# Kernel optimization log

Measured on AMD Instinct MI355X. Metric: run time of the kernel, lower is better.

## Reference

```python
import jax, jax.numpy as jnp
import numpy as np

D_MODEL = 2560
NUM_HEADS = 32
NUM_KV_HEADS = 8
HEAD_DIM = 128
ROPE_THETA = 5e6
EPS = 1e-6
G = NUM_KV_HEADS
Q_PER_KV = NUM_HEADS // NUM_KV_HEADS


def setup_inputs() -> dict:
    key = jax.random.key(0)
    ks = jax.random.split(key, 5)
    B, S = 1, 2048
    scale = 0.02
    return {
        "x": jax.random.normal(ks[0], (B, S, D_MODEL), jnp.float32),
        "Wq": jax.random.normal(ks[1], (NUM_HEADS * HEAD_DIM, D_MODEL), jnp.float32) * scale,
        "Wk": jax.random.normal(ks[2], (NUM_KV_HEADS * HEAD_DIM, D_MODEL), jnp.float32) * scale,
        "Wv": jax.random.normal(ks[3], (NUM_KV_HEADS * HEAD_DIM, D_MODEL), jnp.float32) * scale,
        "Wo": jax.random.normal(ks[4], (D_MODEL, NUM_HEADS * HEAD_DIM), jnp.float32) * scale,
        "q_norm_w": jnp.ones((HEAD_DIM,), jnp.float32),
        "k_norm_w": jnp.ones((HEAD_DIM,), jnp.float32),
    }


def _rms_norm(x, w):
    var = jnp.mean(jnp.square(x), axis=-1, keepdims=True)
    return x * jax.lax.rsqrt(var + EPS) * w


def _rope(x, pos):
    # x: (b, h, s, d); HF-style rotate_half RoPE
    d = x.shape[-1]
    inv_freq = 1.0 / (ROPE_THETA ** (jnp.arange(0, d, 2, dtype=jnp.float32) / d))
    ang = pos[:, None].astype(jnp.float32) * inv_freq[None, :]      # (s, d/2)
    cos = jnp.concatenate([jnp.cos(ang), jnp.cos(ang)], axis=-1)     # (s, d)
    sin = jnp.concatenate([jnp.sin(ang), jnp.sin(ang)], axis=-1)
    x1, x2 = x[..., : d // 2], x[..., d // 2 :]
    rot = jnp.concatenate([-x2, x1], axis=-1)
    return x * cos + rot * sin


def reference(x, Wq, Wk, Wv, Wo, q_norm_w, k_norm_w):
    B, S, _ = x.shape
    pos = jnp.arange(S)
    q = (x @ Wq.T).reshape(B, S, NUM_HEADS, HEAD_DIM).transpose(0, 2, 1, 3)
    k = (x @ Wk.T).reshape(B, S, NUM_KV_HEADS, HEAD_DIM).transpose(0, 2, 1, 3)
    v = (x @ Wv.T).reshape(B, S, NUM_KV_HEADS, HEAD_DIM).transpose(0, 2, 1, 3)
    q = _rope(_rms_norm(q, q_norm_w), pos)
    k = _rope(_rms_norm(k, k_norm_w), pos)
    new_cache_k, new_cache_v = k, v
    # GQA: (b, g, h, s, d) against (b, g, k, d)
    qg = q.reshape(B, G, Q_PER_KV, S, HEAD_DIM)
    scores = jnp.einsum("bghsd,bgkd->bghsk", qg, k) / (HEAD_DIM ** 0.5)
    causal = jnp.triu(jnp.full((S, S), -jnp.inf, jnp.float32), k=1)
    scores = scores + causal
    attn = jax.nn.softmax(scores, axis=-1)
    out = jnp.einsum("bghsk,bgkd->bghsd", attn, v)
    out = out.reshape(B, NUM_HEADS, S, HEAD_DIM).transpose(0, 2, 1, 3).reshape(B, S, NUM_HEADS * HEAD_DIM)
    out = out @ Wo.T
    return (out, new_cache_k, new_cache_v)
```

## Files before the change

kernel.cpp:

```cpp
#include <hip/hip_runtime.h>
#include <hip/hip_bf16.h>
#include <math.h>

#define S_LEN  2048
#define DMODEL 2560
#define NHEADS 32
#define NKV    8
#define HD     128
#define QKDIM  (NHEADS * HD)
#define KVDIM  (NKV * HD)

typedef __bf16 bf16x8 __attribute__((ext_vector_type(8)));
typedef float  f32x4  __attribute__((ext_vector_type(4)));
typedef unsigned short u16;

#define AS1 __attribute__((address_space(1)))
#define AS3 __attribute__((address_space(3)))

__device__ __forceinline__ void load16_to_lds(const void* g, void* l) {
    __builtin_amdgcn_global_load_lds((const AS1 void*)g, (AS3 void*)l, 16, 0, 0);
}

__device__ __forceinline__ u16 f2bf(float f) {
    unsigned u = __builtin_bit_cast(unsigned, f);
    return (u16)((u + 0x7fff + ((u >> 16) & 1)) >> 16);
}

#define PHASE_BAR() do { __builtin_amdgcn_sched_barrier(0);            \
                         __builtin_amdgcn_s_barrier();                 \
                         __builtin_amdgcn_sched_barrier(0); } while (0)
#define WAIT_LGKM0() do { asm volatile("s_waitcnt lgkmcnt(0)" ::: "memory"); \
                          __builtin_amdgcn_sched_barrier(0); } while (0)

__device__ __forceinline__ const bf16x8* fragp(const __bf16* hbase, int row, int colb) {
    int b = (row << 7) | colb;
    b ^= ((b >> 9) & 1) << 5;
    return (const bf16x8*)((const char*)hbase + b);
}

__device__ __forceinline__ void stage_half(const __bf16* __restrict__ g0, int Kp,
                                           __bf16* l0, int wave, int lane) {
#pragma unroll
    for (int j = 0; j < 2; ++j) {
        const int p = ((wave * 2 + j) << 10) | (lane << 4);
        const int b = p ^ (((p >> 9) & 1) << 5);
        load16_to_lds((const char*)g0 + (size_t)(b >> 7) * (Kp * 2) + (b & 127),
                      (char*)l0 + ((wave * 2 + j) << 10));
    }
}

#define N4_X   (S_LEN * DMODEL / 4)
#define N4_WQ  (QKDIM * DMODEL / 4)
#define N4_WK  (KVDIM * DMODEL / 4)
#define N4_ALL (N4_X + N4_WQ + 2 * N4_WK)

__global__ __launch_bounds__(256) void convert_inputs(const float* __restrict__ x,
                                                      const float* __restrict__ wq,
                                                      const float* __restrict__ wk,
                                                      const float* __restrict__ wv,
                                                      u16* __restrict__ xb,
                                                      u16* __restrict__ wb) {
    const int stride = gridDim.x * 256;
    for (int i = blockIdx.x * 256 + threadIdx.x; i < N4_ALL; i += stride) {
        const float4* src;
        ushort4* dst;
        if (i < N4_X) {
            src = (const float4*)x + i;
            dst = (ushort4*)xb + i;
        } else {
            const int j = i - N4_X;
            dst = (ushort4*)wb + j;
            if (j < N4_WQ)                  src = (const float4*)wq + j;
            else if (j < N4_WQ + N4_WK)     src = (const float4*)wk + (j - N4_WQ);
            else                            src = (const float4*)wv + (j - N4_WQ - N4_WK);
        }
        float4 v = *src;
        ushort4 r;
        r.x = f2bf(v.x); r.y = f2bf(v.y); r.z = f2bf(v.z); r.w = f2bf(v.w);
        *dst = r;
    }
}

__global__ __launch_bounds__(256) void f32_to_bf16_k(const float* __restrict__ in,
                                                     u16* __restrict__ out, int n4) {
    int i = blockIdx.x * 256 + threadIdx.x;
    const int stride = gridDim.x * 256;
    for (; i < n4; i += stride) {
        float4 v = ((const float4*)in)[i];
        ushort4 r;
        r.x = f2bf(v.x); r.y = f2bf(v.y); r.z = f2bf(v.z); r.w = f2bf(v.w);
        ((ushort4*)out)[i] = r;
    }
}

__global__ __launch_bounds__(64) void rope_table(float* __restrict__ ct,
                                                 float* __restrict__ st) {
    const int s = blockIdx.x;
    const int i = threadIdx.x;
    const double invf = pow(5.0e6, -(double)i / 64.0);
    const double ang  = (double)s * invf;
    ct[s * 64 + i] = (float)cos(ang);
    st[s * 64 + i] = (float)sin(ang);
}

__global__ __launch_bounds__(256) void gemm_bf16_nt(const __bf16* __restrict__ A,
                                                    const __bf16* __restrict__ B,
                                                    float* __restrict__ C,
                                                    int M, int N, int K) {
    __shared__ __align__(16) __bf16 Als[128 * 64];
    __shared__ __align__(16) __bf16 Bls[128 * 64];
    const int tid  = threadIdx.x;
    const int lane = tid & 63;
    const int wave = tid >> 6;
    const int wm   = wave >> 1, wn = wave & 1;
    const int m0   = blockIdx.y * 128;
    const int n0   = blockIdx.x * 128;
    const int frow = lane & 15;
    const int fkq  = lane >> 4;

    f32x4 acc[4][4];
#pragma unroll
    for (int t = 0; t < 4; ++t)
#pragma unroll
        for (int u = 0; u < 4; ++u)
            acc[t][u] = (f32x4){0.f, 0.f, 0.f, 0.f};

    for (int k0 = 0; k0 < K; k0 += 64) {
        __syncthreads();
#pragma unroll
        for (int i = 0; i < 2; ++i) {
            const int mt  = i * 4 + wave;
            const int row = mt * 16 + frow;
#pragma unroll
            for (int kh = 0; kh < 2; ++kh) {
                const int col = k0 + kh * 32 + fkq * 8;
                load16_to_lds(A + (size_t)(m0 + row) * K + col,
                              &Als[(size_t)((mt * 2 + kh) * 64) * 8]);
                load16_to_lds(B + (size_t)(n0 + row) * K + col,
                              &Bls[(size_t)((mt * 2 + kh) * 64) * 8]);
            }
        }
        __syncthreads();

#pragma unroll
        for (int kh = 0; kh < 2; ++kh) {
            bf16x8 af[4], bfr[4];
#pragma unroll
            for (int t = 0; t < 4; ++t)
                af[t]  = *(const bf16x8*)&Als[(((wm * 4 + t) * 2 + kh) * 64 + lane) * 8];
#pragma unroll
            for (int u = 0; u < 4; ++u)
                bfr[u] = *(const bf16x8*)&Bls[(((wn * 4 + u) * 2 + kh) * 64 + lane) * 8];
#pragma unroll
            for (int t = 0; t < 4; ++t)
#pragma unroll
                for (int u = 0; u < 4; ++u)
                    acc[t][u] = __builtin_amdgcn_mfma_f32_16x16x32_bf16(
                                    af[t], bfr[u], acc[t][u], 0, 0, 0);
        }
    }

    const int crow = (lane >> 4) * 4;
    const int ccol = lane & 15;
#pragma unroll
    for (int t = 0; t < 4; ++t) {
        const int gr = m0 + (wm * 4 + t) * 16 + crow;
#pragma unroll
        for (int u = 0; u < 4; ++u) {
            const int gc = n0 + (wn * 4 + u) * 16 + ccol;
#pragma unroll
            for (int r = 0; r < 4; ++r)
                C[(size_t)(gr + r) * N + gc] = acc[t][u][r];
        }
    }
}

__global__ __launch_bounds__(512, 2) void gemm_qkv_8ph(const __bf16* __restrict__ A,
                                                       const __bf16* __restrict__ Bq,
                                                       const __bf16* __restrict__ Bkv,
                                                       const float* __restrict__ ct,
                                                       const float* __restrict__ st,
                                                       const float* __restrict__ qw,
                                                       const float* __restrict__ kw,
                                                       u16*   __restrict__ qrb,
                                                       float* __restrict__ kc,
                                                       u16*   __restrict__ kcb,
                                                       float* __restrict__ vc,
                                                       u16*   __restrict__ vtb) {
    __shared__ __align__(16) __bf16 Als[4][128 * 64];
    __shared__ __align__(16) __bf16 Bls[4][128 * 64];

    const int K   = DMODEL;
    const int nkt = K / 64;
    const int n0g = blockIdx.x * 256;
    const __bf16* B;
    int n0;
    if (n0g < QKDIM) { B = Bq;  n0 = n0g; }
    else             { B = Bkv; n0 = n0g - QKDIM; }
    const int m0 = blockIdx.y * 256;

    const int tid  = threadIdx.x;
    const int lane = tid & 63;
    const int wave = tid >> 6;
    const int wm   = wave >> 1;
    const int wn   = wave & 1;
    const int frow = lane & 15;
    const int fkq  = lane >> 4;
    const int ha   = wm >> 1;
    const int ar0  = (wm & 1) * 64 + frow;

    f32x4 acc[4][8];
#pragma unroll
    for (int t = 0; t < 4; ++t)
#pragma unroll
        for (int u = 0; u < 8; ++u)
            acc[t][u] = (f32x4){0.f, 0.f, 0.f, 0.f};

    stage_half(A + (size_t)m0 * K,               K, Als[0], wave, lane);
    stage_half(A + (size_t)(m0 + 128) * K,       K, Als[1], wave, lane);
    stage_half(B + (size_t)n0 * K,               K, Bls[0], wave, lane);
    stage_half(B + (size_t)(n0 + 128) * K,       K, Bls[1], wave, lane);
    stage_half(A + (size_t)m0 * K + 64,          K, Als[2], wave, lane);
    stage_half(B + (size_t)n0 * K + 64,          K, Bls[2], wave, lane);
    stage_half(B + (size_t)(n0 + 128) * K + 64,  K, Bls[3], wave, lane);
    asm volatile("s_waitcnt vmcnt(6)" ::: "memory");
    PHASE_BAR();

    for (int kt = 0; kt < nkt; ++kt) {
        const int bf = kt & 1;
        const __bf16* Ahb = Als[bf * 2 + ha];
        const __bf16* Bhb = Bls[bf * 2 + wn];

        bf16x8 a0[2][2], b0[4][2];
#pragma unroll
        for (int mt = 0; mt < 2; ++mt)
#pragma unroll
            for (int kh = 0; kh < 2; ++kh)
                a0[mt][kh] = *fragp(Ahb, ar0 + mt * 16, kh * 64 + fkq * 16);
#pragma unroll
        for (int nt = 0; nt < 4; ++nt)
#pragma unroll
            for (int kh = 0; kh < 2; ++kh)
                b0[nt][kh] = *fragp(Bhb, nt * 16 + frow, kh * 64 + fkq * 16);
        if (kt + 1 < nkt)
            stage_half(A + (size_t)(m0 + 128) * K + (kt + 1) * 64, K,
                       Als[(bf ^ 1) * 2 + 1], wave, lane);
        asm volatile("s_waitcnt lgkmcnt(8)" ::: "memory");
        PHASE_BAR();
        WAIT_LGKM0();
        __builtin_amdgcn_s_setprio(1);
#pragma unroll
        for (int mt = 0; mt < 2; ++mt)
#pragma unroll
            for (int nt = 0; nt < 4; ++nt)
#pragma unroll
                for (int kh = 0; kh < 2; ++kh)
                    acc[mt][nt] = __builtin_amdgcn_mfma_f32_16x16x32_bf16(
                                      a0[mt][kh], b0[nt][kh], acc[mt][nt], 0, 0, 0);
        __builtin_amdgcn_s_setprio(0);
        PHASE_BAR();

        bf16x8 a1[2][2];
#pragma unroll
        for (int mt = 0; mt < 2; ++mt)
#pragma unroll
            for (int kh = 0; kh < 2; ++kh)
                a1[mt][kh] = *fragp(Ahb, ar0 + 32 + mt * 16, kh * 64 + fkq * 16);
        PHASE_BAR();
        WAIT_LGKM0();
        __builtin_amdgcn_s_setprio(1);
#pragma unroll
        for (int mt = 0; mt < 2; ++mt)
#pragma unroll
            for (int nt = 0; nt < 4; ++nt)
#pragma unroll
                for (int kh = 0; kh < 2; ++kh)
                    acc[2 + mt][nt] = __builtin_amdgcn_mfma_f32_16x16x32_bf16(
                                          a1[mt][kh], b0[nt][kh], acc[2 + mt][nt], 0, 0, 0);
        __builtin_amdgcn_s_setprio(0);
        PHASE_BAR();

        bf16x8 b1[4][2];
#pragma unroll
        for (int nt = 0; nt < 4; ++nt)
#pragma unroll
            for (int kh = 0; kh < 2; ++kh)
                b1[nt][kh] = *fragp(Bhb, (4 + nt) * 16 + frow, kh * 64 + fkq * 16);
        if (kt + 2 < nkt)
            stage_half(A + (size_t)m0 * K + (kt + 2) * 64, K,
                       Als[bf * 2 + 0], wave, lane);
        PHASE_BAR();
        WAIT_LGKM0();
        __builtin_amdgcn_s_setprio(1);
#pragma unroll
        for (int mt = 0; mt < 2; ++mt)
#pragma unroll
            for (int nt = 0; nt < 4; ++nt)
#pragma unroll
                for (int kh = 0; kh < 2; ++kh)
                    acc[2 + mt][4 + nt] = __builtin_amdgcn_mfma_f32_16x16x32_bf16(
                                              a1[mt][kh], b1[nt][kh], acc[2 + mt][4 + nt], 0, 0, 0);
        __builtin_amdgcn_s_setprio(0);
        PHASE_BAR();

        if (kt + 2 < nkt) {
            stage_half(B + (size_t)n0 * K + (kt + 2) * 64,         K,
                       Bls[bf * 2 + 0], wave, lane);
            stage_half(B + (size_t)(n0 + 128) * K + (kt + 2) * 64, K,
                       Bls[bf * 2 + 1], wave, lane);
        }
        PHASE_BAR();
        WAIT_LGKM0();
        __builtin_amdgcn_s_setprio(1);
#pragma unroll
        for (int mt = 0; mt < 2; ++mt)
#pragma unroll
            for (int nt = 0; nt < 4; ++nt)
#pragma unroll
                for (int kh = 0; kh < 2; ++kh)
                    acc[mt][4 + nt] = __builtin_amdgcn_mfma_f32_16x16x32_bf16(
                                          a0[mt][kh], b1[nt][kh], acc[mt][4 + nt], 0, 0, 0);
        __builtin_amdgcn_s_setprio(0);
        if (kt < nkt - 2) asm volatile("s_waitcnt vmcnt(6)" ::: "memory");
        else              asm volatile("s_waitcnt vmcnt(0)" ::: "memory");
        PHASE_BAR();
    }

    const int fr = frow;
    const int fq = fkq;
    const int nw = n0g + wn * 128;
    if (n0g < QKDIM + KVDIM) {
        const int isQ = (n0g < QKDIM) ? 1 : 0;
        const float* w = isQ ? qw : kw;
        float wv[8];
#pragma unroll
        for (int u = 0; u < 8; ++u) wv[u] = w[u * 16 + fr];

#pragma unroll
        for (int mt = 0; mt < 4; ++mt) {
#pragma unroll
            for (int r = 0; r < 4; ++r) {
                float ss = 0.f;
#pragma unroll
                for (int u = 0; u < 8; ++u) ss += acc[mt][u][r] * acc[mt][u][r];
                ss += __shfl_xor(ss, 1);
                ss += __shfl_xor(ss, 2);
                ss += __shfl_xor(ss, 4);
                ss += __shfl_xor(ss, 8);
                const float rstd = rsqrtf(ss * (1.0f / 128.0f) + 1e-6f);
                const int s = m0 + wm * 64 + mt * 16 + fq * 4 + r;
#pragma unroll
                for (int u = 0; u < 4; ++u) {
                    const float cs  = ct[s * 64 + u * 16 + fr];
                    const float sn  = st[s * 64 + u * 16 + fr];
                    const float ylo = acc[mt][u][r]     * rstd * wv[u];
                    const float yhi = acc[mt][u + 4][r] * rstd * wv[u + 4];
                    const float olo = ylo * cs - yhi * sn;
                    const float ohi = yhi * cs + ylo * sn;
                    if (isQ) {
                        const int h = nw >> 7;
                        const size_t base = ((size_t)h * S_LEN + s) * HD;
                        qrb[base + u * 16 + fr]       = f2bf(olo * 0.12751743f);
                        qrb[base + (u + 4) * 16 + fr] = f2bf(ohi * 0.12751743f);
                    } else {
                        const int g = (nw - QKDIM) >> 7;
                        const size_t base = ((size_t)g * S_LEN + s) * HD;
                        kc [base + u * 16 + fr]       = olo;
                        kc [base + (u + 4) * 16 + fr] = ohi;
                        kcb[base + u * 16 + fr]       = f2bf(olo);
                        kcb[base + (u + 4) * 16 + fr] = f2bf(ohi);
                    }
                }
            }
        }
    } else {
        const int g = (nw - QKDIM - KVDIM) >> 7;
#pragma unroll
        for (int mt = 0; mt < 4; ++mt) {
            const int sb = m0 + wm * 64 + mt * 16 + fq * 4;
#pragma unroll
            for (int u = 0; u < 8; ++u) {
                const int d = u * 16 + fr;
                ushort4 o;
                o.x = f2bf(acc[mt][u][0]); o.y = f2bf(acc[mt][u][1]);
                o.z = f2bf(acc[mt][u][2]); o.w = f2bf(acc[mt][u][3]);
                *(ushort4*)&vtb[((size_t)g * HD + d) * S_LEN + sb] = o;
#pragma unroll
                for (int r = 0; r < 4; ++r)
                    vc[((size_t)g * S_LEN + sb + r) * HD + d] = acc[mt][u][r];
            }
        }
    }
}

__global__ __launch_bounds__(256, 4) void attn_mfma(const __bf16* __restrict__ Qb,
                                                    const __bf16* __restrict__ Kb,
                                                    const __bf16* __restrict__ Vt,
                                                    u16* __restrict__ Ob) {
    __shared__ __align__(16) __bf16 Kls [4 * 4 * 64 * 8];
    __shared__ __align__(16) __bf16 QVls[8 * 2 * 64 * 8];
    __shared__ __align__(16) __bf16 Pls [4 * 2 * 64 * 8];

    const int h    = blockIdx.x;
    const int g    = h >> 2;
    const int q0   = blockIdx.y * 64;
    const int tid  = threadIdx.x;
    const int lane = tid & 63;
    const int wave = tid >> 6;
    const int fr   = lane & 15;
    const int fq   = lane >> 4;

    {
        const __bf16* Qg = Qb + ((size_t)h * S_LEN + q0 + wave * 16 + fr) * HD;
#pragma unroll
        for (int ks = 0; ks < 4; ++ks)
            load16_to_lds(Qg + ks * 32 + fq * 8, &QVls[(size_t)((wave * 4 + ks) * 64) * 8]);
    }
    __syncthreads();
    bf16x8 aq[4];
#pragma unroll
    for (int ks = 0; ks < 4; ++ks)
        aq[ks] = *(const bf16x8*)&QVls[((wave * 4 + ks) * 64 + lane) * 8];

    float m_i[4], l_i[4];
    f32x4 o_acc[8];
#pragma unroll
    for (int r = 0; r < 4; ++r) { m_i[r] = -INFINITY; l_i[r] = 0.0f; }
#pragma unroll
    for (int dt = 0; dt < 8; ++dt) o_acc[dt] = (f32x4){0.f, 0.f, 0.f, 0.f};

    const int kt_max = blockIdx.y;
    for (int kt = 0; kt <= kt_max; ++kt) {
        __syncthreads();
        {
            const __bf16* Kg = Kb + ((size_t)g * S_LEN + kt * 64 + wave * 16 + fr) * HD;
#pragma unroll
            for (int ks = 0; ks < 4; ++ks)
                load16_to_lds(Kg + ks * 32 + fq * 8, &Kls[(size_t)((wave * 4 + ks) * 64) * 8]);
        }
#pragma unroll
        for (int i = 0; i < 2; ++i) {
            const int dt = wave * 2 + i;
            const __bf16* Vg = Vt + ((size_t)g * HD + dt * 16 + fr) * S_LEN + kt * 64;
#pragma unroll
            for (int ks = 0; ks < 2; ++ks)
                load16_to_lds(Vg + ks * 32 + fq * 8, &QVls[(size_t)((dt * 2 + ks) * 64) * 8]);
        }
        __syncthreads();

        f32x4 s_acc[4];
#pragma unroll
        for (int u = 0; u < 4; ++u) s_acc[u] = (f32x4){0.f, 0.f, 0.f, 0.f};
#pragma unroll
        for (int u = 0; u < 4; ++u)
#pragma unroll
            for (int ks = 0; ks < 4; ++ks)
                s_acc[u] = __builtin_amdgcn_mfma_f32_16x16x32_bf16(
                               aq[ks],
                               *(const bf16x8*)&Kls[((u * 4 + ks) * 64 + lane) * 8],
                               s_acc[u], 0, 0, 0);

        if (kt == kt_max) {
#pragma unroll
            for (int u = 0; u < 4; ++u)
#pragma unroll
                for (int r = 0; r < 4; ++r)
                    if (kt * 64 + u * 16 + fr > q0 + wave * 16 + fq * 4 + r)
                        s_acc[u][r] = -INFINITY;
        }

#pragma unroll
        for (int r = 0; r < 4; ++r) {
            float mx = fmaxf(fmaxf(s_acc[0][r], s_acc[1][r]),
                             fmaxf(s_acc[2][r], s_acc[3][r]));
#pragma unroll
            for (int off = 1; off < 16; off <<= 1)
                mx = fmaxf(mx, __shfl_xor(mx, off));
            const float m_new = fmaxf(m_i[r], mx);
            const float alpha = exp2f(m_i[r] - m_new);
            m_i[r] = m_new;

            float p[4], psum = 0.0f;
#pragma unroll
            for (int u = 0; u < 4; ++u) {
                p[u] = exp2f(s_acc[u][r] - m_new);
                psum += p[u];
            }
#pragma unroll
            for (int off = 1; off < 16; off <<= 1)
                psum += __shfl_xor(psum, off);
            l_i[r] = l_i[r] * alpha + psum;

#pragma unroll
            for (int dt = 0; dt < 8; ++dt) o_acc[dt][r] *= alpha;

#pragma unroll
            for (int u = 0; u < 4; ++u) {
                const int k = u * 16 + fr;
                const int m = fq * 4 + r;
                const int idx = ((wave * 2 + (k >> 5)) * 64 + ((k >> 3) & 3) * 16 + m) * 8
                                + (k & 7);
                ((u16*)Pls)[idx] = f2bf(p[u]);
            }
        }

        bf16x8 ap[2];
#pragma unroll
        for (int ks = 0; ks < 2; ++ks)
            ap[ks] = *(const bf16x8*)&Pls[((wave * 2 + ks) * 64 + lane) * 8];
#pragma unroll
        for (int dt = 0; dt < 8; ++dt)
#pragma unroll
            for (int ks = 0; ks < 2; ++ks)
                o_acc[dt] = __builtin_amdgcn_mfma_f32_16x16x32_bf16(
                                ap[ks],
                                *(const bf16x8*)&QVls[((dt * 2 + ks) * 64 + lane) * 8],
                                o_acc[dt], 0, 0, 0);
    }

#pragma unroll
    for (int r = 0; r < 4; ++r) {
        const float inv_l = 1.0f / l_i[r];
        const int s = q0 + wave * 16 + fq * 4 + r;
#pragma unroll
        for (int dt = 0; dt < 8; ++dt)
            Ob[(size_t)s * QKDIM + h * HD + dt * 16 + fr] = f2bf(o_acc[dt][r] * inv_l);
    }
}

extern "C" void kernel_launch(void* const* d_in, const int* in_sizes, int n_in,
                              void* d_out, int out_size, void* d_ws, size_t ws_size,
                              hipStream_t stream) {
    const float* x  = (const float*)d_in[0];
    const float* Wq = (const float*)d_in[1];
    const float* Wk = (const float*)d_in[2];
    const float* Wv = (const float*)d_in[3];
    const float* Wo = (const float*)d_in[4];
    const float* qw = (const float*)d_in[5];
    const float* kw = (const float*)d_in[6];

    float* out     = (float*)d_out;
    float* cache_k = out + (size_t)S_LEN * DMODEL;
    float* cache_v = cache_k + (size_t)NKV * S_LEN * HD;

    u16* wsu = (u16*)d_ws;
    u16* qrb = wsu;
    u16* kcb = qrb + (size_t)NHEADS * S_LEN * HD;
    u16* vtb = kcb + (size_t)NKV * S_LEN * HD;
    u16* Wqb = vtb + (size_t)NKV * S_LEN * HD;
    u16* Wkb = Wqb + (size_t)QKDIM * DMODEL;
    u16* aob = Wqb;
    u16* Wob = aob + (size_t)S_LEN * QKDIM;
    float* ct = (float*)(Wqb + (size_t)S_LEN * QKDIM + (size_t)DMODEL * QKDIM);
    float* st = ct + S_LEN * 64;
    u16* xb  = (u16*)out;

    convert_inputs<<<4096, 256, 0, stream>>>(x, Wq, Wk, Wv, xb, Wqb);
    rope_table<<<S_LEN, 64, 0, stream>>>(ct, st);

    gemm_qkv_8ph<<<dim3((QKDIM + 2 * KVDIM) / 256, S_LEN / 256), 512, 0, stream>>>(
        (const __bf16*)xb, (const __bf16*)Wqb, (const __bf16*)Wkb,
        ct, st, qw, kw, qrb, cache_k, kcb, cache_v, vtb);

    f32_to_bf16_k<<<1024, 256, 0, stream>>>(Wo, Wob, DMODEL * QKDIM / 4);
    attn_mfma<<<dim3(NHEADS, S_LEN / 64), 256, 0, stream>>>(
        (const __bf16*)qrb, (const __bf16*)kcb, (const __bf16*)vtb, aob);

    gemm_bf16_nt<<<dim3(DMODEL / 128, S_LEN / 128), 256, 0, stream>>>(
        (const __bf16*)aob, (const __bf16*)Wob, out, S_LEN, DMODEL, QKDIM);
}
```

Measured before the change: 503.3 us.

## Pair causal query tiles per block and double-buffer K/V loads in attention

Each attention block now handles two query tiles, a low one and its mirrored high one, so causal work is balanced across blocks and each K/V tile loaded into LDS is reused for both query tiles. K and V tiles are double-buffered, with the next tile's loads issued before the current tile is computed, and s_setprio is raised around the MFMA sections. This targets load latency, redundant K/V traffic and causal load imbalance. In exchange it uses more registers (two accumulator sets) and more LDS, halves the grid, and drops the occupancy hint from launch bounds.

```diff
diff --git a/kernel.cpp b/kernel.cpp
--- a/kernel.cpp
+++ b/kernel.cpp
@@ -393,17 +393,100 @@
     }
 }
 
-__global__ __launch_bounds__(256, 4) void attn_mfma(const __bf16* __restrict__ Qb,
-                                                    const __bf16* __restrict__ Kb,
-                                                    const __bf16* __restrict__ Vt,
-                                                    u16* __restrict__ Ob) {
-    __shared__ __align__(16) __bf16 Kls [4 * 4 * 64 * 8];
-    __shared__ __align__(16) __bf16 QVls[8 * 2 * 64 * 8];
-    __shared__ __align__(16) __bf16 Pls [4 * 2 * 64 * 8];
+__device__ __forceinline__ void attn_tile_compute(
+        const bf16x8 aq[4], f32x4 o_acc[8], float m_i[4], float l_i[4],
+        const __bf16* __restrict__ Kl, const __bf16* __restrict__ Vl,
+        __bf16* __restrict__ Pls, int lane, int wave, int fr, int fq,
+        int qrow0, int kbase, bool diag) {
+    f32x4 s_acc[4];
+#pragma unroll
+    for (int u = 0; u < 4; ++u) s_acc[u] = (f32x4){0.f, 0.f, 0.f, 0.f};
+    __builtin_amdgcn_s_setprio(1);
+#pragma unroll
+    for (int u = 0; u < 4; ++u)
+#pragma unroll
+        for (int ks = 0; ks < 4; ++ks)
+            s_acc[u] = __builtin_amdgcn_mfma_f32_16x16x32_bf16(
+                           aq[ks],
+                           *(const bf16x8*)&Kl[((u * 4 + ks) * 64 + lane) * 8],
+                           s_acc[u], 0, 0, 0);
+    __builtin_amdgcn_s_setprio(0);
+
+    if (diag) {
+#pragma unroll
+        for (int u = 0; u < 4; ++u)
+#pragma unroll
+            for (int r = 0; r < 4; ++r)
+                if (kbase + u * 16 + fr > qrow0 + fq * 4 + r)
+                    s_acc[u][r] = -INFINITY;
+    }
+
+#pragma unroll
+    for (int r = 0; r < 4; ++r) {
+        float mx = fmaxf(fmaxf(s_acc[0][r], s_acc[1][r]),
+                         fmaxf(s_acc[2][r], s_acc[3][r]));
+#pragma unroll
+        for (int off = 1; off < 16; off <<= 1)
+            mx = fmaxf(mx, __shfl_xor(mx, off));
+        const float m_new = fmaxf(m_i[r], mx);
+        const float alpha = exp2f(m_i[r] - m_new);
+        m_i[r] = m_new;
+
+        float p[4], psum = 0.0f;
+#pragma unroll
+        for (int u = 0; u < 4; ++u) {
+            p[u] = exp2f(s_acc[u][r] - m_new);
+            psum += p[u];
+        }
+#pragma unroll
+        for (int off = 1; off < 16; off <<= 1)
+            psum += __shfl_xor(psum, off);
+        l_i[r] = l_i[r] * alpha + psum;
+
+#pragma unroll
+        for (int dt = 0; dt < 8; ++dt) o_acc[dt][r] *= alpha;
+
+#pragma unroll
+        for (int u = 0; u < 4; ++u) {
+            const int k = u * 16 + fr;
+            const int m = fq * 4 + r;
+            const int idx = ((wave * 2 + (k >> 5)) * 64 + ((k >> 3) & 3) * 16 + m) * 8
+                            + (k & 7);
+            ((u16*)Pls)[idx] = f2bf(p[u]);
+        }
+    }
+
+    bf16x8 ap[2];
+#pragma unroll
+    for (int ks = 0; ks < 2; ++ks)
+        ap[ks] = *(const bf16x8*)&Pls[((wave * 2 + ks) * 64 + lane) * 8];
+    __builtin_amdgcn_s_setprio(1);
+#pragma unroll
+    for (int dt = 0; dt < 8; ++dt)
+#pragma unroll
+        for (int ks = 0; ks < 2; ++ks)
+            o_acc[dt] = __builtin_amdgcn_mfma_f32_16x16x32_bf16(
+                            ap[ks],
+                            *(const bf16x8*)&Vl[((dt * 2 + ks) * 64 + lane) * 8],
+                            o_acc[dt], 0, 0, 0);
+    __builtin_amdgcn_s_setprio(0);
+}
+
+__global__ __launch_bounds__(256) void attn_mfma(const __bf16* __restrict__ Qb,
+                                                 const __bf16* __restrict__ Kb,
+                                                 const __bf16* __restrict__ Vt,
+                                                 u16* __restrict__ Ob) {
+    __shared__ __align__(16) __bf16 Kls[2][16 * 64 * 8];
+    __shared__ __align__(16) __bf16 Vls[2][16 * 64 * 8];
+    __shared__ __align__(16) __bf16 Pls[8 * 64 * 8];
 
     const int h    = blockIdx.x;
     const int g    = h >> 2;
-    const int q0   = blockIdx.y * 64;
+    const int pair = blockIdx.y;
+    const int ytl  = pair;
+    const int yth  = (S_LEN / 64 - 1) - pair;
+    const int q0l  = ytl * 64;
+    const int q0h  = yth * 64;
     const int tid  = threadIdx.x;
     const int lane = tid & 63;
     const int wave = tid >> 6;
@@ -411,120 +494,90 @@
     const int fq   = lane >> 4;
 
     {
-        const __bf16* Qg = Qb + ((size_t)h * S_LEN + q0 + wave * 16 + fr) * HD;
+        const __bf16* Qh = Qb + ((size_t)h * S_LEN + q0h + wave * 16 + fr) * HD;
+        const __bf16* Ql = Qb + ((size_t)h * S_LEN + q0l + wave * 16 + fr) * HD;
+#pragma unroll
+        for (int ks = 0; ks < 4; ++ks) {
+            load16_to_lds(Qh + ks * 32 + fq * 8, &Kls[0][(size_t)((wave * 4 + ks) * 64) * 8]);
+            load16_to_lds(Ql + ks * 32 + fq * 8, &Kls[1][(size_t)((wave * 4 + ks) * 64) * 8]);
+        }
+    }
+    __syncthreads();
+    bf16x8 aqh[4], aql[4];
+#pragma unroll
+    for (int ks = 0; ks < 4; ++ks) {
+        aqh[ks] = *(const bf16x8*)&Kls[0][((wave * 4 + ks) * 64 + lane) * 8];
+        aql[ks] = *(const bf16x8*)&Kls[1][((wave * 4 + ks) * 64 + lane) * 8];
+    }
+    __syncthreads();
+
+    float m_h[4], l_h[4], m_l[4], l_l[4];
+    f32x4 o_h[8], o_l[8];
+#pragma unroll
+    for (int r = 0; r < 4; ++r) {
+        m_h[r] = -INFINITY; l_h[r] = 0.0f;
+        m_l[r] = -INFINITY; l_l[r] = 0.0f;
+    }
+#pragma unroll
+    for (int dt = 0; dt < 8; ++dt) {
+        o_h[dt] = (f32x4){0.f, 0.f, 0.f, 0.f};
+        o_l[dt] = (f32x4){0.f, 0.f, 0.f, 0.f};
+    }
+
+    {
+        const __bf16* Kg = Kb + ((size_t)g * S_LEN + wave * 16 + fr) * HD;
 #pragma unroll
         for (int ks = 0; ks < 4; ++ks)
-            load16_to_lds(Qg + ks * 32 + fq * 8, &QVls[(size_t)((wave * 4 + ks) * 64) * 8]);
-    }
-    __syncthreads();
-    bf16x8 aq[4];
-#pragma unroll
-    for (int ks = 0; ks < 4; ++ks)
-        aq[ks] = *(const bf16x8*)&QVls[((wave * 4 + ks) * 64 + lane) * 8];
-
-    float m_i[4], l_i[4];
-    f32x4 o_acc[8];
-#pragma unroll
-    for (int r = 0; r < 4; ++r) { m_i[r] = -INFINITY; l_i[r] = 0.0f; }
-#pragma unroll
-    for (int dt = 0; dt < 8; ++dt) o_acc[dt] = (f32x4){0.f, 0.f, 0.f, 0.f};
-
-    const int kt_max = blockIdx.y;
-    for (int kt = 0; kt <= kt_max; ++kt) {
-        __syncthreads();
-        {
-            const __bf16* Kg = Kb + ((size_t)g * S_LEN + kt * 64 + wave * 16 + fr) * HD;
-#pragma unroll
-            for (int ks = 0; ks < 4; ++ks)
-                load16_to_lds(Kg + ks * 32 + fq * 8, &Kls[(size_t)((wave * 4 + ks) * 64) * 8]);
-        }
+            load16_to_lds(Kg + ks * 32 + fq * 8, &Kls[0][(size_t)((wave * 4 + ks) * 64) * 8]);
 #pragma unroll
         for (int i = 0; i < 2; ++i) {
             const int dt = wave * 2 + i;
-            const __bf16* Vg = Vt + ((size_t)g * HD + dt * 16 + fr) * S_LEN + kt * 64;
+            const __bf16* Vg = Vt + ((size_t)g * HD + dt * 16 + fr) * S_LEN;
 #pragma unroll
             for (int ks = 0; ks < 2; ++ks)
-                load16_to_lds(Vg + ks * 32 + fq * 8, &QVls[(size_t)((dt * 2 + ks) * 64) * 8]);
-        }
+                load16_to_lds(Vg + ks * 32 + fq * 8, &Vls[0][(size_t)((dt * 2 + ks) * 64) * 8]);
+        }
+    }
+    __syncthreads();
+
+    for (int kt = 0; kt <= yth; ++kt) {
+        const int buf = kt & 1;
+        if (kt < yth) {
+            const int nb = buf ^ 1;
+            const __bf16* Kg = Kb + ((size_t)g * S_LEN + (kt + 1) * 64 + wave * 16 + fr) * HD;
+#pragma unroll
+            for (int ks = 0; ks < 4; ++ks)
+                load16_to_lds(Kg + ks * 32 + fq * 8, &Kls[nb][(size_t)((wave * 4 + ks) * 64) * 8]);
+#pragma unroll
+            for (int i = 0; i < 2; ++i) {
+                const int dt = wave * 2 + i;
+                const __bf16* Vg = Vt + ((size_t)g * HD + dt * 16 + fr) * S_LEN + (kt + 1) * 64;
+#pragma unroll
+                for (int ks = 0; ks < 2; ++ks)
+                    load16_to_lds(Vg + ks * 32 + fq * 8, &Vls[nb][(size_t)((dt * 2 + ks) * 64) * 8]);
+            }
+        }
+
+        attn_tile_compute(aqh, o_h, m_h, l_h, Kls[buf], Vls[buf], Pls,
+                          lane, wave, fr, fq, q0h + wave * 16, kt * 64, kt == yth);
+        if (kt <= ytl)
+            attn_tile_compute(aql, o_l, m_l, l_l, Kls[buf], Vls[buf], Pls,
+                              lane, wave, fr, fq, q0l + wave * 16, kt * 64, kt == ytl);
+
         __syncthreads();
-
-        f32x4 s_acc[4];
-#pragma unroll
-        for (int u = 0; u < 4; ++u) s_acc[u] = (f32x4){0.f, 0.f, 0.f, 0.f};
-#pragma unroll
-        for (int u = 0; u < 4; ++u)
-#pragma unroll
-            for (int ks = 0; ks < 4; ++ks)
-                s_acc[u] = __builtin_amdgcn_mfma_f32_16x16x32_bf16(
-                               aq[ks],
-                               *(const bf16x8*)&Kls[((u * 4 + ks) * 64 + lane) * 8],
-                               s_acc[u], 0, 0, 0);
-
-        if (kt == kt_max) {
-#pragma unroll
-            for (int u = 0; u < 4; ++u)
-#pragma unroll
-                for (int r = 0; r < 4; ++r)
-                    if (kt * 64 + u * 16 + fr > q0 + wave * 16 + fq * 4 + r)
-                        s_acc[u][r] = -INFINITY;
-        }
-
-#pragma unroll
-        for (int r = 0; r < 4; ++r) {
-            float mx = fmaxf(fmaxf(s_acc[0][r], s_acc[1][r]),
-                             fmaxf(s_acc[2][r], s_acc[3][r]));
-#pragma unroll
-            for (int off = 1; off < 16; off <<= 1)
-                mx = fmaxf(mx, __shfl_xor(mx, off));
-            const float m_new = fmaxf(m_i[r], mx);
-            const float alpha = exp2f(m_i[r] - m_new);
-            m_i[r] = m_new;
-
-            float p[4], psum = 0.0f;
-#pragma unroll
-            for (int u = 0; u < 4; ++u) {
-                p[u] = exp2f(s_acc[u][r] - m_new);
-                psum += p[u];
-            }
-#pragma unroll
-            for (int off = 1; off < 16; off <<= 1)
-                psum += __shfl_xor(psum, off);
-            l_i[r] = l_i[r] * alpha + psum;
-
-#pragma unroll
-            for (int dt = 0; dt < 8; ++dt) o_acc[dt][r] *= alpha;
-
-#pragma unroll
-            for (int u = 0; u < 4; ++u) {
-                const int k = u * 16 + fr;
-                const int m = fq * 4 + r;
-                const int idx = ((wave * 2 + (k >> 5)) * 64 + ((k >> 3) & 3) * 16 + m) * 8
-                                + (k & 7);
-                ((u16*)Pls)[idx] = f2bf(p[u]);
-            }
-        }
-
-        bf16x8 ap[2];
-#pragma unroll
-        for (int ks = 0; ks < 2; ++ks)
-            ap[ks] = *(const bf16x8*)&Pls[((wave * 2 + ks) * 64 + lane) * 8];
-#pragma unroll
-        for (int dt = 0; dt < 8; ++dt)
-#pragma unroll
-            for (int ks = 0; ks < 2; ++ks)
-                o_acc[dt] = __builtin_amdgcn_mfma_f32_16x16x32_bf16(
-                                ap[ks],
-                                *(const bf16x8*)&QVls[((dt * 2 + ks) * 64 + lane) * 8],
-                                o_acc[dt], 0, 0, 0);
     }
 
 #pragma unroll
     for (int r = 0; r < 4; ++r) {
-        const float inv_l = 1.0f / l_i[r];
-        const int s = q0 + wave * 16 + fq * 4 + r;
-#pragma unroll
-        for (int dt = 0; dt < 8; ++dt)
-            Ob[(size_t)s * QKDIM + h * HD + dt * 16 + fr] = f2bf(o_acc[dt][r] * inv_l);
+        const float ih = 1.0f / l_h[r];
+        const float il = 1.0f / l_l[r];
+        const int sh = q0h + wave * 16 + fq * 4 + r;
+        const int sl = q0l + wave * 16 + fq * 4 + r;
+#pragma unroll
+        for (int dt = 0; dt < 8; ++dt) {
+            Ob[(size_t)sh * QKDIM + h * HD + dt * 16 + fr] = f2bf(o_h[dt][r] * ih);
+            Ob[(size_t)sl * QKDIM + h * HD + dt * 16 + fr] = f2bf(o_l[dt][r] * il);
+        }
     }
 }
 
@@ -563,7 +616,7 @@
         ct, st, qw, kw, qrb, cache_k, kcb, cache_v, vtb);
 
     f32_to_bf16_k<<<1024, 256, 0, stream>>>(Wo, Wob, DMODEL * QKDIM / 4);
-    attn_mfma<<<dim3(NHEADS, S_LEN / 64), 256, 0, stream>>>(
+    attn_mfma<<<dim3(NHEADS, S_LEN / 128), 256, 0, stream>>>(
         (const __bf16*)qrb, (const __bf16*)kcb, (const __bf16*)vtb, aob);
 
     gemm_bf16_nt<<<dim3(DMODEL / 128, S_LEN / 128), 256, 0, stream>>>(
```

New measurement: 484.9 us. -3.7%, faster.
